# Kernel optimization log

Hardware: AMD Instinct MI355X
Metric: run time of the kernel (lower is better)

Reference implementation:

```python
import jax, jax.numpy as jnp
import numpy as np

D_MODEL = 1024
N_HEAD = 16
N_KV = 8
HEAD_DIM = D_MODEL // N_HEAD  # 64
ROPE_BASE = 10000.0


def _rope_tables(T, head_dim):
    inv_freq = 1.0 / (ROPE_BASE ** (jnp.arange(0, head_dim, 2, dtype=jnp.float32) / head_dim))
    pos = jnp.arange(T, dtype=jnp.float32)
    freqs = pos[:, None] * inv_freq[None, :]  # [T, head_dim//2]
    return jnp.sin(freqs), jnp.cos(freqs)


def _apply_rope(x, sin, cos):
    # x: [B, H, T, D]; sin/cos: [T, D//2] broadcast over B,H
    x1 = x[..., ::2]
    x2 = x[..., 1::2]
    y1 = x1 * cos - x2 * sin
    y2 = x1 * sin + x2 * cos
    return jnp.stack([y1, y2], axis=-1).reshape(x.shape)


def setup_inputs() -> dict:
    key = jax.random.key(0)
    ks = jax.random.split(key, 5)
    B, T = 2, 2048
    x = jax.random.normal(ks[0], (B, T, D_MODEL), dtype=jnp.float32)
    std = 0.02
    Wq = std * jax.random.normal(ks[1], (D_MODEL, D_MODEL), dtype=jnp.float32)
    Wk = std * jax.random.normal(ks[2], (N_KV * HEAD_DIM, D_MODEL), dtype=jnp.float32)
    Wv = std * jax.random.normal(ks[3], (N_KV * HEAD_DIM, D_MODEL), dtype=jnp.float32)
    Wo = std * jax.random.normal(ks[4], (D_MODEL, D_MODEL), dtype=jnp.float32)
    return {"x": x, "Wq": Wq, "Wk": Wk, "Wv": Wv, "Wo": Wo}


def reference(x, Wq, Wk, Wv, Wo):
    B, T, _ = x.shape
    G = N_HEAD // N_KV  # query heads per kv head (repeat_interleave grouping)

    # projections (bias-free Linear: x @ W.T)
    q = (x @ Wq.T).reshape(B, T, N_HEAD, HEAD_DIM).transpose(0, 2, 1, 3)  # [B,H,T,D]
    k = (x @ Wk.T).reshape(B, T, N_KV, HEAD_DIM).transpose(0, 2, 1, 3)   # [B,Hkv,T,D]
    v = (x @ Wv.T).reshape(B, T, N_KV, HEAD_DIM).transpose(0, 2, 1, 3)

    sin, cos = _rope_tables(T, HEAD_DIM)
    q = _apply_rope(q, sin, cos)
    k = _apply_rope(k, sin, cos)

    # GQA without materializing repeated K/V: group q heads by kv head.
    # repeat_interleave(dim=1) maps q head h -> kv head h // G.
    qg = q.reshape(B, N_KV, G, T, HEAD_DIM)
    scale = 1.0 / np.sqrt(HEAD_DIM)
    scores = jnp.einsum('bkgtd,bksd->bkgts', qg, k) * scale  # [B,Hkv,G,T,T]
    causal = jnp.tril(jnp.ones((T, T), dtype=bool))
    scores = jnp.where(causal, scores, jnp.float32(-1e30))
    attn = jax.nn.softmax(scores, axis=-1)
    y = jnp.einsum('bkgts,bksd->bkgtd', attn, v)              # [B,Hkv,G,T,D]
    y = y.reshape(B, N_HEAD, T, HEAD_DIM).transpose(0, 2, 1, 3).reshape(B, T, D_MODEL)
    return y @ Wo.T
```

## Files before the change

### kernel.cpp

```cpp
#include <hip/hip_runtime.h>
#include <cstdint>
#include <cstddef>

typedef __attribute__((ext_vector_type(8))) __bf16 bf16x8;
typedef __attribute__((ext_vector_type(4))) __bf16 bf16x4;
typedef __attribute__((ext_vector_type(4))) float f32x4;

#define DEVI __device__ __forceinline__

DEVI void gload_lds16(const void* g, void* l) {
    __builtin_amdgcn_global_load_lds((const __attribute__((address_space(1))) void*)g,
                                     (__attribute__((address_space(3))) void*)l, 16, 0, 0);
}

__global__ __launch_bounds__(256) void cvt_all(
    const float* __restrict__ x, const float* __restrict__ wq,
    const float* __restrict__ wk, const float* __restrict__ wv,
    const float* __restrict__ wo,
    bf16x4* __restrict__ xb, bf16x4* __restrict__ wqb, bf16x4* __restrict__ wkb,
    bf16x4* __restrict__ wvb, bf16x4* __restrict__ wob)
{
    int i = blockIdx.x * 256 + threadIdx.x;
    const int stride = gridDim.x * 256;
    for (; i < 1835008; i += stride) {
        const float4* s; bf16x4* d; int j;
        if (i < 1048576)      { s = (const float4*)x;  d = xb;  j = i; }
        else if (i < 1310720) { s = (const float4*)wq; d = wqb; j = i - 1048576; }
        else if (i < 1441792) { s = (const float4*)wk; d = wkb; j = i - 1310720; }
        else if (i < 1572864) { s = (const float4*)wv; d = wvb; j = i - 1441792; }
        else                  { s = (const float4*)wo; d = wob; j = i - 1572864; }
        float4 v = s[j];
        bf16x4 o = { (__bf16)v.x, (__bf16)v.y, (__bf16)v.z, (__bf16)v.w };
        d[j] = o;
    }
}

__global__ __launch_bounds__(256) void rope_tables(float* __restrict__ sint, float* __restrict__ cost)
{
    int i = blockIdx.x * 256 + threadIdx.x;
    int t = i >> 5, p = i & 31;
    float inv = powf(10000.0f, -(float)p / 32.0f);
    float f = (float)t * inv;
    float s, c;
    sincosf(f, &s, &c);
    sint[i] = s;
    cost[i] = c;
}

__global__ __launch_bounds__(256) void qkv_gemm(
    const __bf16* __restrict__ xb, const __bf16* __restrict__ wqb,
    const __bf16* __restrict__ wkb, const __bf16* __restrict__ wvb,
    const float* __restrict__ sint, const float* __restrict__ cost,
    __bf16* __restrict__ Qo, __bf16* __restrict__ Ko, __bf16* __restrict__ Vo)
{
    __shared__ __bf16 As[2][4096];
    __shared__ __bf16 Bs[2][4096];
    const int tid = threadIdx.x;
    const int lane = tid & 63;
    const int wid = tid >> 6;
    const int wm = (wid >> 1) * 32, wn = (wid & 1) * 32;
    const int m0 = blockIdx.y * 64;
    const int n0 = blockIdx.x * 64;

    const __bf16* bsrc;
    if (n0 < 1024)      bsrc = wqb + (size_t)n0 * 1024;
    else if (n0 < 1536) bsrc = wkb + (size_t)(n0 - 1024) * 1024;
    else                bsrc = wvb + (size_t)(n0 - 1536) * 1024;
    const __bf16* asrc = xb + (size_t)m0 * 1024;

    f32x4 acc[2][2] = {};
    const int sr = tid >> 3, sc = tid & 7;
    const int gsc = (sc ^ (sr & 7)) * 8;

#define STAGE(BUF, K0) do {                                                             \
    gload_lds16(asrc + (size_t)sr * 1024 + (K0) + gsc,        (char*)As[BUF] + sr * 128 + sc * 16); \
    gload_lds16(asrc + (size_t)(sr + 32) * 1024 + (K0) + gsc, (char*)As[BUF] + (sr + 32) * 128 + sc * 16); \
    gload_lds16(bsrc + (size_t)sr * 1024 + (K0) + gsc,        (char*)Bs[BUF] + sr * 128 + sc * 16); \
    gload_lds16(bsrc + (size_t)(sr + 32) * 1024 + (K0) + gsc, (char*)Bs[BUF] + (sr + 32) * 128 + sc * 16); \
} while (0)

    STAGE(0, 0);
    __syncthreads();

#pragma unroll 1
    for (int step = 0; step < 16; ++step) {
        const int cur = step & 1;
        if (step < 15) STAGE(cur ^ 1, (step + 1) * 64);
#pragma unroll
        for (int ks = 0; ks < 2; ++ks) {
            bf16x8 af[2], bfv[2];
#pragma unroll
            for (int i = 0; i < 2; ++i) {
                int ra = wm + i * 16 + (lane & 15);
                af[i] = *(const bf16x8*)((const char*)As[cur] + ra * 128 + (((ks * 4 + (lane >> 4)) ^ (ra & 7)) * 16));
                int rb = wn + i * 16 + (lane & 15);
                bfv[i] = *(const bf16x8*)((const char*)Bs[cur] + rb * 128 + (((ks * 4 + (lane >> 4)) ^ (rb & 7)) * 16));
            }
#pragma unroll
            for (int mi = 0; mi < 2; ++mi)
#pragma unroll
                for (int ni = 0; ni < 2; ++ni)
                    acc[mi][ni] = __builtin_amdgcn_mfma_f32_16x16x32_bf16(af[mi], bfv[ni], acc[mi][ni], 0, 0, 0);
        }
        __syncthreads();
    }
#undef STAGE

    const int rg = lane >> 4, cf = lane & 15;
#pragma unroll
    for (int mi = 0; mi < 2; ++mi) {
#pragma unroll
        for (int ni = 0; ni < 2; ++ni) {
#pragma unroll
            for (int r = 0; r < 4; ++r) {
                float v = acc[mi][ni][r];
                float pv = __shfl_xor(v, 1, 64);
                int m = m0 + wm + mi * 16 + rg * 4 + r;
                int n = n0 + wn + ni * 16 + cf;
                int b = m >> 11;
                int t = m & 2047;
                if (n < 1024) {
                    int h = n >> 6, d = n & 63;
                    float s = sint[t * 32 + (d >> 1)], c = cost[t * 32 + (d >> 1)];
                    float o = (d & 1) ? (pv * s + v * c) : (v * c - pv * s);
                    Qo[((size_t)(b * 16 + h) * 2048 + t) * 64 + d] = (__bf16)(o * 0.125f);
                } else if (n < 1536) {
                    int nn = n - 1024;
                    int h = nn >> 6, d = nn & 63;
                    float s = sint[t * 32 + (d >> 1)], c = cost[t * 32 + (d >> 1)];
                    float o = (d & 1) ? (pv * s + v * c) : (v * c - pv * s);
                    Ko[((size_t)(b * 8 + h) * 2048 + t) * 64 + d] = (__bf16)o;
                } else {
                    int nn = n - 1536;
                    int h = nn >> 6, d = nn & 63;
                    Vo[((size_t)(b * 8 + h) * 2048 + t) * 64 + d] = (__bf16)v;
                }
            }
        }
    }
}

__global__ __launch_bounds__(256) void v_transpose(const __bf16* __restrict__ Vg, __bf16* __restrict__ VTg)
{
    __shared__ __bf16 tile[64][72];
    const int tid = threadIdx.x;
    const int t0 = blockIdx.x * 64;
    const int bh = blockIdx.y;
    const size_t base = (size_t)bh * 2048 * 64;
    const int rr = tid >> 3, c8 = (tid & 7) * 8;
#pragma unroll
    for (int it = 0; it < 2; ++it) {
        int tt = rr + it * 32;
        *(bf16x8*)(&tile[tt][c8]) = *(const bf16x8*)(Vg + base + (size_t)(t0 + tt) * 64 + c8);
    }
    __syncthreads();
#pragma unroll
    for (int it = 0; it < 2; ++it) {
        int d = rr + it * 32;
        bf16x8 o;
#pragma unroll
        for (int j = 0; j < 8; ++j) o[j] = tile[c8 + j][d];
        *(bf16x8*)(VTg + base + (size_t)d * 2048 + t0 + c8) = o;
    }
}

__global__ __launch_bounds__(256, 2) void attn_fwd(
    const __bf16* __restrict__ Qg, const __bf16* __restrict__ Kg,
    const __bf16* __restrict__ VTg, __bf16* __restrict__ Yg)
{
    __shared__ char Ks[2][8192];
    __shared__ char Vs[2][8192];
    __shared__ char Pl[8192];
    const int tid = threadIdx.x;
    const int lane = tid & 63;
    const int w = tid >> 6;
    const int lin = blockIdx.x;
    const int xcd = lin & 7, g = (lin >> 3) & 3, p = lin >> 5;
    const int bh = xcd + 8 * g;
    const int b = bh >> 4, h = bh & 15, kvh = h >> 1;
    const size_t qbase = (size_t)(b * 16 + h) * 2048 * 64;
    const size_t kbase = (size_t)(b * 8 + kvh) * 2048 * 64;
    const int rg = lane >> 4, cf = lane & 15;
    char* pw = Pl + w * 2048;

    const int sr = tid >> 3;
    const int sc = tid & 7;
    const int gsc = (sc ^ (sr & 7)) * 8;

    const int Ja = p, Jb = 31 - p;
    bf16x8 pk0, pk1, pv0, pv1;

    bf16x8 ones;
#pragma unroll
    for (int e = 0; e < 8; ++e) ones[e] = (__bf16)1.0f;

#define PRE(NT) do {                                                                    \
    const int _n0 = (NT) * 64;                                                          \
    pk0 = *(const bf16x8*)(Kg + kbase + (size_t)(_n0 + sr) * 64 + gsc);                 \
    pk1 = *(const bf16x8*)(Kg + kbase + (size_t)(_n0 + sr + 32) * 64 + gsc);            \
    pv0 = *(const bf16x8*)(VTg + kbase + (size_t)sr * 2048 + _n0 + gsc);                \
    pv1 = *(const bf16x8*)(VTg + kbase + (size_t)(sr + 32) * 2048 + _n0 + gsc);         \
} while (0)
#define WRITE_LDS(BUF) do {                                                             \
    *(bf16x8*)(Ks[BUF] + tid * 16) = pk0;                                               \
    *(bf16x8*)(Ks[BUF] + (tid + 256) * 16) = pk1;                                       \
    *(bf16x8*)(Vs[BUF] + tid * 16) = pv0;                                               \
    *(bf16x8*)(Vs[BUF] + (tid + 256) * 16) = pv1;                                       \
} while (0)

    PRE(0);
    WRITE_LDS(0);
    __syncthreads();

    bf16x8 qf[2];
    f32x4 oacc[4], lacc;
    int J = Ja, nt = 0, cur = 0;

#pragma unroll 1
    for (int s = 0; s <= 32; ++s) {
        const int r0 = J * 64 + w * 16;
        if (nt == 0) {
#pragma unroll
            for (int ks = 0; ks < 2; ++ks)
                qf[ks] = *(const bf16x8*)(Qg + qbase + (size_t)(r0 + cf) * 64 + ks * 32 + rg * 8);
#pragma unroll
            for (int r = 0; r < 4; ++r) oacc[r] = f32x4{};
            lacc = f32x4{};
        }

        if (s < 32) {
            const int nnt = (nt == J) ? 0 : nt + 1;
            PRE(nnt);
        }

        {
            bf16x8 kf[2][4];
#pragma unroll
            for (int ks = 0; ks < 2; ++ks)
#pragma unroll
                for (int ni = 0; ni < 4; ++ni)
                    kf[ks][ni] = *(const bf16x8*)(Ks[cur] + (ni * 16 + cf) * 128 + (((ks * 4 + rg) ^ (cf & 7)) * 16));

            f32x4 sacc[4] = {};
            __builtin_amdgcn_s_setprio(1);
#pragma unroll
            for (int ks = 0; ks < 2; ++ks)
#pragma unroll
                for (int ni = 0; ni < 4; ++ni)
                    sacc[ni] = __builtin_amdgcn_mfma_f32_16x16x32_bf16(qf[ks], kf[ks][ni], sacc[ni], 0, 0, 0);
            __builtin_amdgcn_s_setprio(0);

            bf16x8 vf[2][4];
#pragma unroll
            for (int ks = 0; ks < 2; ++ks)
#pragma unroll
                for (int df = 0; df < 4; ++df)
                    vf[ks][df] = *(const bf16x8*)(Vs[cur] + (df * 16 + cf) * 128 + (((ks * 4 + rg) ^ (cf & 7)) * 16));

            if (nt == J) {
#pragma unroll
                for (int ni = 0; ni < 4; ++ni)
#pragma unroll
                    for (int r = 0; r < 4; ++r)
                        if (ni * 16 + cf > w * 16 + rg * 4 + r)
                            sacc[ni][r] = -3.0e38f;
            }

#pragma unroll
            for (int ni = 0; ni < 4; ++ni)
#pragma unroll
                for (int r = 0; r < 4; ++r)
                    sacc[ni][r] = __expf(sacc[ni][r]);

#pragma unroll
            for (int ni = 0; ni < 4; ++ni)
#pragma unroll
                for (int r = 0; r < 4; ++r) {
                    int pr = rg * 4 + r;
                    int pc = ni * 16 + cf;
                    *(__bf16*)(pw + pr * 128 + (((pc >> 3) ^ (pr & 7)) * 8 + (pc & 7)) * 2) =
                        (__bf16)sacc[ni][r];
                }

            __builtin_amdgcn_s_setprio(1);
#pragma unroll
            for (int ks = 0; ks < 2; ++ks) {
                bf16x8 pf = *(const bf16x8*)(pw + cf * 128 + (((ks * 4 + rg) ^ (cf & 7)) * 16));
#pragma unroll
                for (int df = 0; df < 4; ++df)
                    oacc[df] = __builtin_amdgcn_mfma_f32_16x16x32_bf16(pf, vf[ks][df], oacc[df], 0, 0, 0);
                lacc = __builtin_amdgcn_mfma_f32_16x16x32_bf16(pf, ones, lacc, 0, 0, 0);
            }
            __builtin_amdgcn_s_setprio(0);
        }

        if (nt == J) {
#pragma unroll
            for (int r = 0; r < 4; ++r) {
                float inv = 1.0f / lacc[r];
                int t = r0 + rg * 4 + r;
#pragma unroll
                for (int df = 0; df < 4; ++df)
                    Yg[((size_t)b * 2048 + t) * 1024 + h * 64 + df * 16 + cf] =
                        (__bf16)(oacc[df][r] * inv);
            }
        }

        if (s < 32) WRITE_LDS(cur ^ 1);
        __syncthreads();
        cur ^= 1;
        if (nt == J) { J = Jb; nt = 0; } else ++nt;
    }
#undef PRE
#undef WRITE_LDS
}

__global__ __launch_bounds__(256) void out_gemm(
    const __bf16* __restrict__ Yb, const __bf16* __restrict__ Wob, float* __restrict__ outp)
{
    __shared__ __bf16 As[2][8192];
    __shared__ __bf16 Bs[2][4096];
    const int tid = threadIdx.x;
    const int lane = tid & 63;
    const int wid = tid >> 6;
    const int wm = wid * 32;
    const int m0 = blockIdx.y * 128;
    const int n0 = blockIdx.x * 64;
    const __bf16* asrc = Yb + (size_t)m0 * 1024;
    const __bf16* bsrc = Wob + (size_t)n0 * 1024;

    f32x4 acc[2][4] = {};
    const int srow = tid >> 3, schunk = tid & 7;
    const int gc = (schunk ^ (srow & 7)) * 8;

#define STAGE(BUF, K0) do {                                                             \
    _Pragma("unroll") for (int it = 0; it < 4; ++it) {                                  \
        int r = srow + it * 32;                                                         \
        gload_lds16(asrc + (size_t)r * 1024 + (K0) + gc, (char*)As[BUF] + r * 128 + schunk * 16); \
    }                                                                                   \
    _Pragma("unroll") for (int it = 0; it < 2; ++it) {                                  \
        int r = srow + it * 32;                                                         \
        gload_lds16(bsrc + (size_t)r * 1024 + (K0) + gc, (char*)Bs[BUF] + r * 128 + schunk * 16); \
    }                                                                                   \
} while (0)

    STAGE(0, 0);
    __syncthreads();

#pragma unroll 1
    for (int step = 0; step < 16; ++step) {
        const int cur = step & 1;
        if (step < 15) STAGE(cur ^ 1, (step + 1) * 64);
#pragma unroll
        for (int ks = 0; ks < 2; ++ks) {
            bf16x8 af[2], bfv[4];
#pragma unroll
            for (int i = 0; i < 2; ++i) {
                int ra = wm + i * 16 + (lane & 15);
                af[i] = *(const bf16x8*)((const char*)As[cur] + ra * 128 + (((ks * 4 + (lane >> 4)) ^ (ra & 7)) * 16));
            }
#pragma unroll
            for (int i = 0; i < 4; ++i) {
                int rb = i * 16 + (lane & 15);
                bfv[i] = *(const bf16x8*)((const char*)Bs[cur] + rb * 128 + (((ks * 4 + (lane >> 4)) ^ (rb & 7)) * 16));
            }
#pragma unroll
            for (int mi = 0; mi < 2; ++mi)
#pragma unroll
                for (int ni = 0; ni < 4; ++ni)
                    acc[mi][ni] = __builtin_amdgcn_mfma_f32_16x16x32_bf16(af[mi], bfv[ni], acc[mi][ni], 0, 0, 0);
        }
        __syncthreads();
    }
#undef STAGE

    const int rg = lane >> 4, cf = lane & 15;
#pragma unroll
    for (int mi = 0; mi < 2; ++mi)
#pragma unroll
        for (int ni = 0; ni < 4; ++ni)
#pragma unroll
            for (int r = 0; r < 4; ++r) {
                int m = m0 + wm + mi * 16 + rg * 4 + r;
                int n = n0 + ni * 16 + cf;
                outp[(size_t)m * 1024 + n] = acc[mi][ni][r];
            }
}

extern "C" void kernel_launch(void* const* d_in, const int* in_sizes, int n_in,
                              void* d_out, int out_size, void* d_ws, size_t ws_size,
                              hipStream_t stream)
{
    const float* x  = (const float*)d_in[0];
    const float* wq = (const float*)d_in[1];
    const float* wk = (const float*)d_in[2];
    const float* wv = (const float*)d_in[3];
    const float* wo = (const float*)d_in[4];

    char* ws = (char*)d_ws;
    __bf16* xb  = (__bf16*)(ws + 0);
    __bf16* wqb = (__bf16*)(ws + 8388608);
    __bf16* wkb = (__bf16*)(ws + 10485760);
    __bf16* wvb = (__bf16*)(ws + 11534336);
    __bf16* wob = (__bf16*)(ws + 12582912);
    __bf16* Qb  = (__bf16*)(ws + 14680064);
    __bf16* Kb  = (__bf16*)(ws + 23068672);
    __bf16* Vb  = (__bf16*)(ws + 27262976);
    __bf16* VTb = (__bf16*)(ws + 31457280);
    __bf16* Yb  = (__bf16*)(ws + 35651584);
    float* sint = (float*)(ws + 44040192);
    float* cost = (float*)(ws + 44302336);
    if (ws_size < 44564480) return;

    cvt_all<<<2048, 256, 0, stream>>>(x, wq, wk, wv, wo,
                                      (bf16x4*)xb, (bf16x4*)wqb, (bf16x4*)wkb,
                                      (bf16x4*)wvb, (bf16x4*)wob);
    rope_tables<<<256, 256, 0, stream>>>(sint, cost);
    qkv_gemm<<<dim3(32, 64), 256, 0, stream>>>(xb, wqb, wkb, wvb, sint, cost, Qb, Kb, Vb);
    v_transpose<<<dim3(32, 16), 256, 0, stream>>>(Vb, VTb);
    attn_fwd<<<512, 256, 0, stream>>>(Qb, Kb, VTb, Yb);
    out_gemm<<<dim3(16, 32), 256, 0, stream>>>(Yb, wob, (float*)d_out);
}
```

Measured before the change: 109.3 us.

## Process both paired query tiles in one KV sweep to share K/V loads

The attention kernel now handles its two causal-balanced query tiles (p and 31-p) at the same time, streaming KV tiles once from 0 to J2 and reusing each loaded K/V tile for both query tiles while nt <= J1. Before, it swept KV twice, once per query tile, so the shared prefix tiles were loaded again. In exchange each thread holds two sets of accumulators and Q fragments, LDS use grows by a second P buffer, and the occupancy hint of 2 blocks per CU is dropped, which may reduce occupancy.

```diff
diff --git a/kernel.cpp b/kernel.cpp
--- a/kernel.cpp
+++ b/kernel.cpp
@@ -164,13 +164,14 @@
     }
 }
 
-__global__ __launch_bounds__(256, 2) void attn_fwd(
+__global__ __launch_bounds__(256) void attn_fwd(
     const __bf16* __restrict__ Qg, const __bf16* __restrict__ Kg,
     const __bf16* __restrict__ VTg, __bf16* __restrict__ Yg)
 {
     __shared__ char Ks[2][8192];
     __shared__ char Vs[2][8192];
-    __shared__ char Pl[8192];
+    __shared__ char P1[8192];
+    __shared__ char P2[8192];
     const int tid = threadIdx.x;
     const int lane = tid & 63;
     const int w = tid >> 6;
@@ -181,13 +182,14 @@
     const size_t qbase = (size_t)(b * 16 + h) * 2048 * 64;
     const size_t kbase = (size_t)(b * 8 + kvh) * 2048 * 64;
     const int rg = lane >> 4, cf = lane & 15;
-    char* pw = Pl + w * 2048;
+    char* pw1 = P1 + w * 2048;
+    char* pw2 = P2 + w * 2048;
 
     const int sr = tid >> 3;
     const int sc = tid & 7;
     const int gsc = (sc ^ (sr & 7)) * 8;
 
-    const int Ja = p, Jb = 31 - p;
+    const int J1 = p, J2 = 31 - p;
     bf16x8 pk0, pk1, pv0, pv1;
 
     bf16x8 ones;
@@ -208,108 +210,140 @@
     *(bf16x8*)(Vs[BUF] + (tid + 256) * 16) = pv1;                                       \
 } while (0)
 
+    bf16x8 qf1[2], qf2[2];
+#pragma unroll
+    for (int ks = 0; ks < 2; ++ks) {
+        qf1[ks] = *(const bf16x8*)(Qg + qbase + (size_t)(J1 * 64 + w * 16 + cf) * 64 + ks * 32 + rg * 8);
+        qf2[ks] = *(const bf16x8*)(Qg + qbase + (size_t)(J2 * 64 + w * 16 + cf) * 64 + ks * 32 + rg * 8);
+    }
+    f32x4 oacc1[4] = {}, oacc2[4] = {}, lacc1 = {}, lacc2 = {};
+
     PRE(0);
     WRITE_LDS(0);
     __syncthreads();
 
-    bf16x8 qf[2];
-    f32x4 oacc[4], lacc;
-    int J = Ja, nt = 0, cur = 0;
-
 #pragma unroll 1
-    for (int s = 0; s <= 32; ++s) {
-        const int r0 = J * 64 + w * 16;
-        if (nt == 0) {
+    for (int nt = 0; nt <= J2; ++nt) {
+        const int cur = nt & 1;
+        if (nt < J2) PRE(nt + 1);
+        const bool a1 = (nt <= J1);
+
+        bf16x8 kf[2][4];
+#pragma unroll
+        for (int ks = 0; ks < 2; ++ks)
+#pragma unroll
+            for (int ni = 0; ni < 4; ++ni)
+                kf[ks][ni] = *(const bf16x8*)(Ks[cur] + (ni * 16 + cf) * 128 + (((ks * 4 + rg) ^ (cf & 7)) * 16));
+
+        f32x4 s2[4] = {}, s1[4] = {};
+        __builtin_amdgcn_s_setprio(1);
+#pragma unroll
+        for (int ks = 0; ks < 2; ++ks)
+#pragma unroll
+            for (int ni = 0; ni < 4; ++ni)
+                s2[ni] = __builtin_amdgcn_mfma_f32_16x16x32_bf16(qf2[ks], kf[ks][ni], s2[ni], 0, 0, 0);
+        if (a1) {
 #pragma unroll
             for (int ks = 0; ks < 2; ++ks)
-                qf[ks] = *(const bf16x8*)(Qg + qbase + (size_t)(r0 + cf) * 64 + ks * 32 + rg * 8);
-#pragma unroll
-            for (int r = 0; r < 4; ++r) oacc[r] = f32x4{};
-            lacc = f32x4{};
-        }
-
-        if (s < 32) {
-            const int nnt = (nt == J) ? 0 : nt + 1;
-            PRE(nnt);
-        }
-
-        {
-            bf16x8 kf[2][4];
-#pragma unroll
-            for (int ks = 0; ks < 2; ++ks)
 #pragma unroll
                 for (int ni = 0; ni < 4; ++ni)
-                    kf[ks][ni] = *(const bf16x8*)(Ks[cur] + (ni * 16 + cf) * 128 + (((ks * 4 + rg) ^ (cf & 7)) * 16));
-
-            f32x4 sacc[4] = {};
-            __builtin_amdgcn_s_setprio(1);
-#pragma unroll
-            for (int ks = 0; ks < 2; ++ks)
-#pragma unroll
-                for (int ni = 0; ni < 4; ++ni)
-                    sacc[ni] = __builtin_amdgcn_mfma_f32_16x16x32_bf16(qf[ks], kf[ks][ni], sacc[ni], 0, 0, 0);
-            __builtin_amdgcn_s_setprio(0);
-
-            bf16x8 vf[2][4];
-#pragma unroll
-            for (int ks = 0; ks < 2; ++ks)
+                    s1[ni] = __builtin_amdgcn_mfma_f32_16x16x32_bf16(qf1[ks], kf[ks][ni], s1[ni], 0, 0, 0);
+        }
+        __builtin_amdgcn_s_setprio(0);
+
+        bf16x8 vf[2][4];
+#pragma unroll
+        for (int ks = 0; ks < 2; ++ks)
+#pragma unroll
+            for (int df = 0; df < 4; ++df)
+                vf[ks][df] = *(const bf16x8*)(Vs[cur] + (df * 16 + cf) * 128 + (((ks * 4 + rg) ^ (cf & 7)) * 16));
+
+        if (nt == J1) {
+#pragma unroll
+            for (int ni = 0; ni < 4; ++ni)
+#pragma unroll
+                for (int r = 0; r < 4; ++r)
+                    if (ni * 16 + cf > w * 16 + rg * 4 + r)
+                        s1[ni][r] = -3.0e38f;
+        }
+        if (nt == J2) {
+#pragma unroll
+            for (int ni = 0; ni < 4; ++ni)
+#pragma unroll
+                for (int r = 0; r < 4; ++r)
+                    if (ni * 16 + cf > w * 16 + rg * 4 + r)
+                        s2[ni][r] = -3.0e38f;
+        }
+
+#pragma unroll
+        for (int ni = 0; ni < 4; ++ni)
+#pragma unroll
+            for (int r = 0; r < 4; ++r)
+                s2[ni][r] = __expf(s2[ni][r]);
+        if (a1) {
+#pragma unroll
+            for (int ni = 0; ni < 4; ++ni)
+#pragma unroll
+                for (int r = 0; r < 4; ++r)
+                    s1[ni][r] = __expf(s1[ni][r]);
+        }
+
+#pragma unroll
+        for (int ni = 0; ni < 4; ++ni)
+#pragma unroll
+            for (int r = 0; r < 4; ++r) {
+                int pr = rg * 4 + r;
+                int pc = ni * 16 + cf;
+                int off = pr * 128 + (((pc >> 3) ^ (pr & 7)) * 8 + (pc & 7)) * 2;
+                *(__bf16*)(pw2 + off) = (__bf16)s2[ni][r];
+                if (a1) *(__bf16*)(pw1 + off) = (__bf16)s1[ni][r];
+            }
+
+        __builtin_amdgcn_s_setprio(1);
+#pragma unroll
+        for (int ks = 0; ks < 2; ++ks) {
+            bf16x8 pf2 = *(const bf16x8*)(pw2 + cf * 128 + (((ks * 4 + rg) ^ (cf & 7)) * 16));
+#pragma unroll
+            for (int df = 0; df < 4; ++df)
+                oacc2[df] = __builtin_amdgcn_mfma_f32_16x16x32_bf16(pf2, vf[ks][df], oacc2[df], 0, 0, 0);
+            lacc2 = __builtin_amdgcn_mfma_f32_16x16x32_bf16(pf2, ones, lacc2, 0, 0, 0);
+        }
+        if (a1) {
+#pragma unroll
+            for (int ks = 0; ks < 2; ++ks) {
+                bf16x8 pf1 = *(const bf16x8*)(pw1 + cf * 128 + (((ks * 4 + rg) ^ (cf & 7)) * 16));
 #pragma unroll
                 for (int df = 0; df < 4; ++df)
-                    vf[ks][df] = *(const bf16x8*)(Vs[cur] + (df * 16 + cf) * 128 + (((ks * 4 + rg) ^ (cf & 7)) * 16));
-
-            if (nt == J) {
-#pragma unroll
-                for (int ni = 0; ni < 4; ++ni)
-#pragma unroll
-                    for (int r = 0; r < 4; ++r)
-                        if (ni * 16 + cf > w * 16 + rg * 4 + r)
-                            sacc[ni][r] = -3.0e38f;
-            }
-
-#pragma unroll
-            for (int ni = 0; ni < 4; ++ni)
-#pragma unroll
-                for (int r = 0; r < 4; ++r)
-                    sacc[ni][r] = __expf(sacc[ni][r]);
-
-#pragma unroll
-            for (int ni = 0; ni < 4; ++ni)
-#pragma unroll
-                for (int r = 0; r < 4; ++r) {
-                    int pr = rg * 4 + r;
-                    int pc = ni * 16 + cf;
-                    *(__bf16*)(pw + pr * 128 + (((pc >> 3) ^ (pr & 7)) * 8 + (pc & 7)) * 2) =
-                        (__bf16)sacc[ni][r];
-                }
-
-            __builtin_amdgcn_s_setprio(1);
-#pragma unroll
-            for (int ks = 0; ks < 2; ++ks) {
-                bf16x8 pf = *(const bf16x8*)(pw + cf * 128 + (((ks * 4 + rg) ^ (cf & 7)) * 16));
-#pragma unroll
-                for (int df = 0; df < 4; ++df)
-                    oacc[df] = __builtin_amdgcn_mfma_f32_16x16x32_bf16(pf, vf[ks][df], oacc[df], 0, 0, 0);
-                lacc = __builtin_amdgcn_mfma_f32_16x16x32_bf16(pf, ones, lacc, 0, 0, 0);
-            }
-            __builtin_amdgcn_s_setprio(0);
-        }
-
-        if (nt == J) {
+                    oacc1[df] = __builtin_amdgcn_mfma_f32_16x16x32_bf16(pf1, vf[ks][df], oacc1[df], 0, 0, 0);
+                lacc1 = __builtin_amdgcn_mfma_f32_16x16x32_bf16(pf1, ones, lacc1, 0, 0, 0);
+            }
+        }
+        __builtin_amdgcn_s_setprio(0);
+
+        if (nt == J1) {
 #pragma unroll
             for (int r = 0; r < 4; ++r) {
-                float inv = 1.0f / lacc[r];
-                int t = r0 + rg * 4 + r;
+                float inv = 1.0f / lacc1[r];
+                int t = J1 * 64 + w * 16 + rg * 4 + r;
 #pragma unroll
                 for (int df = 0; df < 4; ++df)
                     Yg[((size_t)b * 2048 + t) * 1024 + h * 64 + df * 16 + cf] =
-                        (__bf16)(oacc[df][r] * inv);
-            }
-        }
-
-        if (s < 32) WRITE_LDS(cur ^ 1);
+                        (__bf16)(oacc1[df][r] * inv);
+            }
+        }
+
+        if (nt < J2) WRITE_LDS(cur ^ 1);
         __syncthreads();
-        cur ^= 1;
-        if (nt == J) { J = Jb; nt = 0; } else ++nt;
+    }
+
+#pragma unroll
+    for (int r = 0; r < 4; ++r) {
+        float inv = 1.0f / lacc2[r];
+        int t = J2 * 64 + w * 16 + rg * 4 + r;
+#pragma unroll
+        for (int df = 0; df < 4; ++df)
+            Yg[((size_t)b * 2048 + t) * 1024 + h * 64 + df * 16 + cf] =
+                (__bf16)(oacc2[df][r] * inv);
     }
 #undef PRE
 #undef WRITE_LDS
```

Result: slower. 120.4 us (+10.2%).
